# Kernel optimization log

Hardware: AMD Instinct MI355X
Metric: run time of the kernel (lower is better)

Reference implementation:

```python
import jax, jax.numpy as jnp
import numpy as np

B, S, H, F, E, TOP_K = 4, 2048, 768, 3072, 8, 2


def setup_inputs() -> dict:
    key = jax.random.key(0)
    ks = jax.random.split(key, 6)
    x = jax.random.normal(ks[0], (B, S, H), dtype=jnp.float32)
    Wr = jax.random.normal(ks[1], (E, H), dtype=jnp.float32) * 0.02
    Wi = jax.random.normal(ks[2], (E, F, H), dtype=jnp.float32) * 0.02
    bi = jnp.zeros((E, F), dtype=jnp.float32)
    Wo = jax.random.normal(ks[3], (E, H, F), dtype=jnp.float32) * 0.02
    bo = jnp.zeros((E, H), dtype=jnp.float32)
    return {"x": x, "Wr": Wr, "Wi": Wi, "bi": bi, "Wo": Wo, "bo": bo}


def reference(x, Wr, Wi, bi, Wo, bo):
    # x: [B, S, H] -> tokens [T, H]
    xf = x.reshape(-1, x.shape[-1])  # [T, H]

    # Router: linear (no bias), eval mode (no noise), temperature=1.0
    router_logits = jnp.einsum('th,eh->te', xf, Wr)  # [T, E]
    topk_vals, topk_idx = jax.lax.top_k(router_logits, TOP_K)  # [T, K]
    routing_weights = jax.nn.softmax(topk_vals, axis=-1)  # normalize over top-k

    # All experts on all tokens (forward_all_experts, parallel computation)
    h = jnp.einsum('th,efh->etf', xf, Wi) + bi[:, None, :]  # [E, T, F]
    h = jax.nn.gelu(h, approximate=False)  # BERT gelu (erf)
    expert_out = jnp.einsum('etf,ehf->eth', h, Wo) + bo[:, None, :]  # [E, T, H]
    expert_out = jnp.transpose(expert_out, (1, 0, 2))  # [T, E, H]

    # Gather top-k expert outputs per token and combine with routing weights
    gathered = jnp.take_along_axis(expert_out, topk_idx[:, :, None], axis=1)  # [T, K, H]
    out = jnp.einsum('tk,tkh->th', routing_weights, gathered)
    return out.reshape(x.shape)
```

## Files before the change

kernel.cpp:

```cpp
#include <hip/hip_runtime.h>
#include <hip/hip_bf16.h>
#include <cstdint>
#include <cstddef>

#define T_TOK 8192
#define HDIM  768
#define FDIM  3072
#define NEXP  8

typedef __attribute__((ext_vector_type(8))) __bf16 bf16x8;
typedef __attribute__((ext_vector_type(4))) float  f32x4;

static __device__ __forceinline__ f32x4 mfma16(bf16x8 a, bf16x8 b, f32x4 c) {
  return __builtin_amdgcn_mfma_f32_16x16x32_bf16(a, b, c, 0, 0, 0);
}

static __device__ __forceinline__ unsigned short f2b(float f) {
  return __builtin_bit_cast(unsigned short, (__bf16)f);
}

static constexpr size_t OFF_XB   = 0;
static constexpr size_t OFF_WIB  = OFF_XB  + (size_t)T_TOK * HDIM * 2;
static constexpr size_t OFF_WOB  = OFF_WIB + (size_t)NEXP * FDIM * HDIM * 2;
static constexpr size_t OFF_HBUF = OFF_WOB + (size_t)NEXP * HDIM * FDIM * 2;
static constexpr size_t OFF_META = OFF_HBUF + (size_t)2 * T_TOK * FDIM * 2;
static constexpr size_t OFF_TOKE = OFF_META + 256;
static constexpr size_t OFF_TOKW = OFF_TOKE + 65536;
static constexpr size_t OFF_PTOK = OFF_TOKW + 65536;
static constexpr size_t OFF_PW   = OFF_PTOK + 65536;
static constexpr size_t OFF_STAGE = 0;

__global__ __launch_bounds__(256) void cvt_kernel(const float* __restrict__ s,
                                                  unsigned short* __restrict__ d, int n4) {
  int i = blockIdx.x * 256 + threadIdx.x;
  int stride = gridDim.x * 256;
  for (; i < n4; i += stride) {
    float4 v = ((const float4*)s)[i];
    ushort4 o;
    o.x = f2b(v.x); o.y = f2b(v.y); o.z = f2b(v.z); o.w = f2b(v.w);
    ((ushort4*)d)[i] = o;
  }
}

__global__ __launch_bounds__(256) void router_kernel(const float* __restrict__ x,
                                                     const float* __restrict__ Wr,
                                                     int* __restrict__ tok_e,
                                                     float* __restrict__ tok_w) {
  __shared__ float wr[NEXP * HDIM];
  int tid = threadIdx.x;
  for (int i = tid; i < NEXP * HDIM; i += 256) wr[i] = Wr[i];
  __syncthreads();
  int lane = tid & 63;
  int wv = tid >> 6;
  int t = blockIdx.x * 4 + wv;
  const float* xr = x + (size_t)t * HDIM;
  float p[NEXP];
#pragma unroll
  for (int e = 0; e < NEXP; ++e) p[e] = 0.f;
  for (int j = 0; j < HDIM / 64; ++j) {
    float xv = xr[j * 64 + lane];
#pragma unroll
    for (int e = 0; e < NEXP; ++e) p[e] += xv * wr[e * HDIM + j * 64 + lane];
  }
#pragma unroll
  for (int e = 0; e < NEXP; ++e) {
    float v = p[e];
    for (int off = 32; off; off >>= 1) v += __shfl_xor(v, off);
    p[e] = v;
  }
  if (lane == 0) {
    float v0 = -1e30f, v1 = -1e30f; int i0 = 0, i1 = 0;
#pragma unroll
    for (int e = 0; e < NEXP; ++e) {
      float v = p[e];
      if (v > v0) { v1 = v0; i1 = i0; v0 = v; i0 = e; }
      else if (v > v1) { v1 = v; i1 = e; }
    }
    float ew = expf(v1 - v0);
    float w0 = 1.0f / (1.0f + ew);
    float w1 = ew * w0;
    tok_e[t * 2 + 0] = i0; tok_w[t * 2 + 0] = w0;
    tok_e[t * 2 + 1] = i1; tok_w[t * 2 + 1] = w1;
  }
}

__global__ __launch_bounds__(256) void count_kernel(const int* __restrict__ tok_e,
                                                    int* __restrict__ counts) {
  __shared__ int h[NEXP];
  int tid = threadIdx.x;
  if (tid < NEXP) h[tid] = 0;
  __syncthreads();
  int i = blockIdx.x * 256 + tid;
  atomicAdd(&h[tok_e[i]], 1);
  __syncthreads();
  if (tid < NEXP && h[tid] > 0) atomicAdd(&counts[tid], h[tid]);
}

__global__ void scan_kernel(const int* __restrict__ counts, int* __restrict__ base) {
  if (threadIdx.x == 0 && blockIdx.x == 0) {
    int s = 0;
    for (int e = 0; e < NEXP; ++e) { base[e] = s; s += counts[e]; }
  }
}

__global__ __launch_bounds__(256) void scatter_kernel(const int* __restrict__ tok_e,
                                                      const float* __restrict__ tok_w,
                                                      const int* __restrict__ base,
                                                      int* __restrict__ cursor,
                                                      int* __restrict__ pair_tok,
                                                      float* __restrict__ pair_w) {
  __shared__ int h[NEXP], bstart[NEXP];
  int tid = threadIdx.x;
  if (tid < NEXP) h[tid] = 0;
  __syncthreads();
  int i = blockIdx.x * 256 + tid;
  int e = tok_e[i];
  int r = atomicAdd(&h[e], 1);
  __syncthreads();
  if (tid < NEXP) bstart[tid] = (h[tid] > 0) ? atomicAdd(&cursor[tid], h[tid]) : 0;
  __syncthreads();
  int pos = base[e] + bstart[e] + r;
  pair_tok[pos] = i;
  pair_w[pos] = tok_w[i];
}

template <int MODE>
__global__ __launch_bounds__(512, 2) void moe_gemm(
    const unsigned short* __restrict__ abase,
    const unsigned short* __restrict__ wbase,
    const float* __restrict__ bias,
    const int* __restrict__ counts, const int* __restrict__ base,
    const int* __restrict__ pair_tok, const float* __restrict__ pair_w,
    unsigned short* __restrict__ hbuf, float* __restrict__ stage) {
  constexpr int K  = MODE ? FDIM : HDIM;
  constexpr int N  = MODE ? HDIM : FDIM;
  constexpr int NT = K / 64;

  const int e = blockIdx.z;
  const int ne = counts[e];
  const int mt = blockIdx.y;
  if (mt * 256 >= ne) return;
  const int nt = blockIdx.x;
  const int pb = base[e];

  extern __shared__ char smem[];

  const int tid = threadIdx.x;
  const int lane = tid & 63;
  const int wv = tid >> 6;
  const int wm = wv >> 2;
  const int wn = wv & 3;
  const int l15 = lane & 15;
  const int lkb = (lane >> 4) * 16;

  const int crow = tid >> 3;
  const int ck = tid & 7;
  const int swz = (ck ^ (crow & 7)) * 16;
  const char* aS[4]; const char* bS[4];
#pragma unroll
  for (int i = 0; i < 4; ++i) {
    int gr = mt * 256 + i * 64 + crow; if (gr > ne - 1) gr = ne - 1;
    if constexpr (MODE == 0) {
      int tok = pair_tok[pb + gr] >> 1;
      aS[i] = (const char*)abase + (size_t)tok * (HDIM * 2) + swz;
    } else {
      aS[i] = (const char*)abase + (size_t)(pb + gr) * (FDIM * 2) + swz;
    }
    int br = nt * 256 + i * 64 + crow;
    bS[i] = (const char*)wbase + ((size_t)e * N * K + (size_t)br * K) * 2 + swz;
  }

  auto STAGE = [&](int c, int t) {
    if (t < NT) {
      const char* src = (c < 4 ? aS[c] : bS[c - 4]) + t * 128;
      char* dst = smem + (size_t)((t & 1) * 65536 + c * 8192 + tid * 16);
      __builtin_amdgcn_global_load_lds(
          (const __attribute__((address_space(1))) void*)src,
          (__attribute__((address_space(3))) void*)dst, 16, 0, 0);
    }
  };

  bf16x8 aR[8], bR0[4], bR1[4];
  f32x4 acc[8][4];
#pragma unroll
  for (int mi = 0; mi < 8; ++mi)
#pragma unroll
    for (int ni = 0; ni < 4; ++ni) acc[mi][ni] = (f32x4){0.f, 0.f, 0.f, 0.f};

  auto READA = [&](int cb, int h) {
#pragma unroll
    for (int m2 = 0; m2 < 4; ++m2)
#pragma unroll
      for (int k2 = 0; k2 < 2; ++k2) {
        int lr = wm * 128 + (h * 4 + m2) * 16 + l15;
        int cbyte = k2 * 64 + lkb;
        aR[m2 * 2 + k2] =
            *(const bf16x8*)(smem + cb + lr * 128 + (cbyte ^ ((lr & 7) << 4)));
      }
  };
  auto READB = [&](int cb, int h, bf16x8* bR) {
#pragma unroll
    for (int n2 = 0; n2 < 2; ++n2)
#pragma unroll
      for (int k2 = 0; k2 < 2; ++k2) {
        int lr = wn * 64 + (h * 2 + n2) * 16 + l15;
        int cbyte = k2 * 64 + lkb;
        bR[n2 * 2 + k2] =
            *(const bf16x8*)(smem + cb + 32768 + lr * 128 + (cbyte ^ ((lr & 7) << 4)));
      }
  };
  auto MFMAQ = [&](int qm, int qn, const bf16x8* bR) {
#pragma unroll
    for (int m2 = 0; m2 < 4; ++m2)
#pragma unroll
      for (int n2 = 0; n2 < 2; ++n2)
#pragma unroll
        for (int k2 = 0; k2 < 2; ++k2)
          acc[qm * 4 + m2][qn * 2 + n2] =
              mfma16(aR[m2 * 2 + k2], bR[n2 * 2 + k2], acc[qm * 4 + m2][qn * 2 + n2]);
  };

#pragma unroll
  for (int c = 0; c < 8; ++c) STAGE(c, 0);
  STAGE(0, 1); STAGE(1, 1);
  asm volatile("s_waitcnt vmcnt(2)" ::: "memory");
  __builtin_amdgcn_s_barrier();

  for (int t = 0; t < NT; ++t) {
    const int cb = (t & 1) * 65536;
    READA(cb, 0); READB(cb, 0, bR0);
    STAGE(2, t + 1); STAGE(3, t + 1);
    __builtin_amdgcn_s_barrier();
    asm volatile("s_waitcnt lgkmcnt(0)" ::: "memory");
    __builtin_amdgcn_sched_barrier(0);
    __builtin_amdgcn_s_setprio(1);
    MFMAQ(0, 0, bR0);
    __builtin_amdgcn_s_setprio(0);
    __builtin_amdgcn_s_barrier();
    READB(cb, 1, bR1);
    STAGE(4, t + 1); STAGE(5, t + 1);
    __builtin_amdgcn_s_barrier();
    asm volatile("s_waitcnt lgkmcnt(0)" ::: "memory");
    __builtin_amdgcn_sched_barrier(0);
    __builtin_amdgcn_s_setprio(1);
    MFMAQ(0, 1, bR1);
    __builtin_amdgcn_s_setprio(0);
    __builtin_amdgcn_s_barrier();
    READA(cb, 1);
    STAGE(6, t + 1); STAGE(7, t + 1);
    __builtin_amdgcn_s_barrier();
    asm volatile("s_waitcnt lgkmcnt(0)" ::: "memory");
    __builtin_amdgcn_sched_barrier(0);
    __builtin_amdgcn_s_setprio(1);
    MFMAQ(1, 1, bR1);
    __builtin_amdgcn_s_setprio(0);
    __builtin_amdgcn_s_barrier();
    STAGE(0, t + 2); STAGE(1, t + 2);
    __builtin_amdgcn_s_barrier();
    __builtin_amdgcn_s_setprio(1);
    MFMAQ(1, 0, bR0);
    __builtin_amdgcn_s_setprio(0);
    if (t + 2 < NT) asm volatile("s_waitcnt vmcnt(2)" ::: "memory");
    else            asm volatile("s_waitcnt vmcnt(0)" ::: "memory");
    __builtin_amdgcn_s_barrier();
  }

  if constexpr (MODE == 0) {
    const float* be = bias + (size_t)e * FDIM;
    float bv[4];
#pragma unroll
    for (int ni = 0; ni < 4; ++ni) bv[ni] = be[nt * 256 + wn * 64 + ni * 16 + l15];
#pragma unroll
    for (int mi = 0; mi < 8; ++mi)
#pragma unroll
      for (int r = 0; r < 4; ++r) {
        int row = mt * 256 + wm * 128 + mi * 16 + (lane >> 4) * 4 + r;
        if (row < ne) {
          unsigned short* hr = hbuf + (size_t)(pb + row) * FDIM + nt * 256 + wn * 64 + l15;
#pragma unroll
          for (int ni = 0; ni < 4; ++ni) {
            float v = acc[mi][ni][r] + bv[ni];
            v = 0.5f * v * (1.0f + erff(v * 0.70710678118654752f));
            hr[ni * 16] = f2b(v);
          }
        }
      }
  } else {
    const float* be = bias + (size_t)e * HDIM;
    float bv[4];
#pragma unroll
    for (int ni = 0; ni < 4; ++ni) bv[ni] = be[nt * 256 + wn * 64 + ni * 16 + l15];
#pragma unroll
    for (int mi = 0; mi < 8; ++mi)
#pragma unroll
      for (int r = 0; r < 4; ++r) {
        int row = mt * 256 + wm * 128 + mi * 16 + (lane >> 4) * 4 + r;
        if (row < ne) {
          int p = pb + row;
          int ts = pair_tok[p];
          float w = pair_w[p];
          float* sr = stage + (size_t)ts * HDIM + nt * 256 + wn * 64 + l15;
#pragma unroll
          for (int ni = 0; ni < 4; ++ni)
            sr[ni * 16] = (acc[mi][ni][r] + bv[ni]) * w;
        }
      }
  }
}

__global__ __launch_bounds__(256) void combine_kernel(const float* __restrict__ stage,
                                                      float* __restrict__ out) {
  const int n4 = T_TOK * HDIM / 4;
  int i = blockIdx.x * 256 + threadIdx.x;
  int stride = gridDim.x * 256;
  const float4* s = (const float4*)stage;
  float4* o = (float4*)out;
  for (; i < n4; i += stride) {
    int t = i / (HDIM / 4);
    int h = i - t * (HDIM / 4);
    float4 a = s[(size_t)t * (HDIM / 2) + h];
    float4 b = s[(size_t)t * (HDIM / 2) + (HDIM / 4) + h];
    float4 r; r.x = a.x + b.x; r.y = a.y + b.y; r.z = a.z + b.z; r.w = a.w + b.w;
    o[i] = r;
  }
}

extern "C" void kernel_launch(void* const* d_in, const int* in_sizes, int n_in,
                              void* d_out, int out_size, void* d_ws, size_t ws_size,
                              hipStream_t stream) {
  const float* x  = (const float*)d_in[0];
  const float* Wr = (const float*)d_in[1];
  const float* Wi = (const float*)d_in[2];
  const float* bi = (const float*)d_in[3];
  const float* Wo = (const float*)d_in[4];
  const float* bo = (const float*)d_in[5];
  float* out = (float*)d_out;
  char* ws = (char*)d_ws;

  unsigned short* xb   = (unsigned short*)(ws + OFF_XB);
  unsigned short* wib  = (unsigned short*)(ws + OFF_WIB);
  unsigned short* wob  = (unsigned short*)(ws + OFF_WOB);
  unsigned short* hbuf = (unsigned short*)(ws + OFF_HBUF);
  int*   counts   = (int*)(ws + OFF_META);
  int*   basep    = (int*)(ws + OFF_META + 64);
  int*   cursor   = (int*)(ws + OFF_META + 128);
  int*   tok_e    = (int*)(ws + OFF_TOKE);
  float* tok_w    = (float*)(ws + OFF_TOKW);
  int*   pair_tok = (int*)(ws + OFF_PTOK);
  float* pair_w   = (float*)(ws + OFF_PW);
  float* stage    = (float*)(ws + OFF_STAGE);

  hipFuncSetAttribute((const void*)&moe_gemm<0>,
                      hipFuncAttributeMaxDynamicSharedMemorySize, 131072);
  hipFuncSetAttribute((const void*)&moe_gemm<1>,
                      hipFuncAttributeMaxDynamicSharedMemorySize, 131072);

  hipMemsetAsync(ws + OFF_META, 0, 256, stream);

  cvt_kernel<<<1024, 256, 0, stream>>>(x, xb, T_TOK * HDIM / 4);
  cvt_kernel<<<2048, 256, 0, stream>>>(Wi, wib, NEXP * FDIM * HDIM / 4);
  cvt_kernel<<<2048, 256, 0, stream>>>(Wo, wob, NEXP * HDIM * FDIM / 4);

  router_kernel<<<T_TOK / 4, 256, 0, stream>>>(x, Wr, tok_e, tok_w);
  count_kernel<<<64, 256, 0, stream>>>(tok_e, counts);
  scan_kernel<<<1, 64, 0, stream>>>(counts, basep);
  scatter_kernel<<<64, 256, 0, stream>>>(tok_e, tok_w, basep, cursor, pair_tok, pair_w);

  moe_gemm<0><<<dim3(FDIM / 256, T_TOK / 256, NEXP), 512, 131072, stream>>>(
      xb, wib, bi, counts, basep, pair_tok, pair_w, hbuf, nullptr);
  moe_gemm<1><<<dim3(HDIM / 256, T_TOK / 256, NEXP), 512, 131072, stream>>>(
      hbuf, wob, bo, counts, basep, pair_tok, pair_w, nullptr, stage);

  combine_kernel<<<2048, 256, 0, stream>>>(stage, out);
}
```

Before: 332.6 us.

## Split MoE GEMM into specialized kernels with 256x192 tiles and swizzled block order

Replaces the templated grouped GEMM with two dedicated kernels. The down-projection now uses 256x192 output tiles, so each expert gets four N tiles instead of three and more workgroups run on the many-CU GPU. It uses a reduced shared-memory footprint and a new MFMA schedule split into 2+1 column subgroups. Both kernels use 1-D grids with experts interleaved and M tiles grouped for L2 reuse of weights and activations. The cost is a narrower N tile with less reuse of A per block and a more complex pipeline.

```diff
diff --git a/kernel.cpp b/kernel.cpp
--- a/kernel.cpp
+++ b/kernel.cpp
@@ -17,6 +17,12 @@
 
 static __device__ __forceinline__ unsigned short f2b(float f) {
   return __builtin_bit_cast(unsigned short, (__bf16)f);
+}
+
+static __device__ __forceinline__ void gload16(const void* g, void* l) {
+  __builtin_amdgcn_global_load_lds(
+      (const __attribute__((address_space(1))) void*)g,
+      (__attribute__((address_space(3))) void*)l, 16, 0, 0);
 }
 
 static constexpr size_t OFF_XB   = 0;
@@ -124,24 +130,22 @@
   pair_w[pos] = tok_w[i];
 }
 
-template <int MODE>
-__global__ __launch_bounds__(512, 2) void moe_gemm(
-    const unsigned short* __restrict__ abase,
-    const unsigned short* __restrict__ wbase,
-    const float* __restrict__ bias,
+__global__ __launch_bounds__(512, 2) void gemmA_kernel(
+    const unsigned short* __restrict__ xb, const unsigned short* __restrict__ wib,
+    const float* __restrict__ bi,
     const int* __restrict__ counts, const int* __restrict__ base,
-    const int* __restrict__ pair_tok, const float* __restrict__ pair_w,
-    unsigned short* __restrict__ hbuf, float* __restrict__ stage) {
-  constexpr int K  = MODE ? FDIM : HDIM;
-  constexpr int N  = MODE ? HDIM : FDIM;
-  constexpr int NT = K / 64;
-
-  const int e = blockIdx.z;
+    const int* __restrict__ pair_tok, unsigned short* __restrict__ hbuf) {
+  const int bid = blockIdx.x;
+  const int e = bid & 7;
+  const int j = bid >> 3;
+  const int mtq = j / 48;
+  const int rem = j - mtq * 48;
+  const int nt = rem >> 2;
+  const int mt = mtq * 4 + (rem & 3);
   const int ne = counts[e];
-  const int mt = blockIdx.y;
   if (mt * 256 >= ne) return;
-  const int nt = blockIdx.x;
   const int pb = base[e];
+  constexpr int NT = HDIM / 64;
 
   extern __shared__ char smem[];
 
@@ -160,23 +164,17 @@
 #pragma unroll
   for (int i = 0; i < 4; ++i) {
     int gr = mt * 256 + i * 64 + crow; if (gr > ne - 1) gr = ne - 1;
-    if constexpr (MODE == 0) {
-      int tok = pair_tok[pb + gr] >> 1;
-      aS[i] = (const char*)abase + (size_t)tok * (HDIM * 2) + swz;
-    } else {
-      aS[i] = (const char*)abase + (size_t)(pb + gr) * (FDIM * 2) + swz;
-    }
+    int tok = pair_tok[pb + gr] >> 1;
+    aS[i] = (const char*)xb + (size_t)tok * (HDIM * 2) + swz;
     int br = nt * 256 + i * 64 + crow;
-    bS[i] = (const char*)wbase + ((size_t)e * N * K + (size_t)br * K) * 2 + swz;
+    bS[i] = (const char*)wib + ((size_t)e * FDIM * HDIM + (size_t)br * HDIM) * 2 + swz;
   }
 
   auto STAGE = [&](int c, int t) {
     if (t < NT) {
       const char* src = (c < 4 ? aS[c] : bS[c - 4]) + t * 128;
       char* dst = smem + (size_t)((t & 1) * 65536 + c * 8192 + tid * 16);
-      __builtin_amdgcn_global_load_lds(
-          (const __attribute__((address_space(1))) void*)src,
-          (__attribute__((address_space(3))) void*)dst, 16, 0, 0);
+      gload16(src, dst);
     }
   };
 
@@ -265,47 +263,196 @@
     __builtin_amdgcn_s_barrier();
   }
 
-  if constexpr (MODE == 0) {
-    const float* be = bias + (size_t)e * FDIM;
-    float bv[4];
-#pragma unroll
-    for (int ni = 0; ni < 4; ++ni) bv[ni] = be[nt * 256 + wn * 64 + ni * 16 + l15];
-#pragma unroll
-    for (int mi = 0; mi < 8; ++mi)
-#pragma unroll
-      for (int r = 0; r < 4; ++r) {
-        int row = mt * 256 + wm * 128 + mi * 16 + (lane >> 4) * 4 + r;
-        if (row < ne) {
-          unsigned short* hr = hbuf + (size_t)(pb + row) * FDIM + nt * 256 + wn * 64 + l15;
-#pragma unroll
-          for (int ni = 0; ni < 4; ++ni) {
-            float v = acc[mi][ni][r] + bv[ni];
-            v = 0.5f * v * (1.0f + erff(v * 0.70710678118654752f));
-            hr[ni * 16] = f2b(v);
-          }
+  const float* be = bi + (size_t)e * FDIM;
+  float bv[4];
+#pragma unroll
+  for (int ni = 0; ni < 4; ++ni) bv[ni] = be[nt * 256 + wn * 64 + ni * 16 + l15];
+#pragma unroll
+  for (int mi = 0; mi < 8; ++mi)
+#pragma unroll
+    for (int r = 0; r < 4; ++r) {
+      int row = mt * 256 + wm * 128 + mi * 16 + (lane >> 4) * 4 + r;
+      if (row < ne) {
+        unsigned short* hr = hbuf + (size_t)(pb + row) * FDIM + nt * 256 + wn * 64 + l15;
+#pragma unroll
+        for (int ni = 0; ni < 4; ++ni) {
+          float v = acc[mi][ni][r] + bv[ni];
+          v = 0.5f * v * (1.0f + erff(v * 0.70710678118654752f));
+          hr[ni * 16] = f2b(v);
         }
       }
-  } else {
-    const float* be = bias + (size_t)e * HDIM;
-    float bv[4];
-#pragma unroll
-    for (int ni = 0; ni < 4; ++ni) bv[ni] = be[nt * 256 + wn * 64 + ni * 16 + l15];
-#pragma unroll
-    for (int mi = 0; mi < 8; ++mi)
-#pragma unroll
-      for (int r = 0; r < 4; ++r) {
-        int row = mt * 256 + wm * 128 + mi * 16 + (lane >> 4) * 4 + r;
-        if (row < ne) {
-          int p = pb + row;
-          int ts = pair_tok[p];
-          float w = pair_w[p];
-          float* sr = stage + (size_t)ts * HDIM + nt * 256 + wn * 64 + l15;
-#pragma unroll
-          for (int ni = 0; ni < 4; ++ni)
-            sr[ni * 16] = (acc[mi][ni][r] + bv[ni]) * w;
-        }
+    }
+}
+
+__global__ __launch_bounds__(512, 2) void gemmB_kernel(
+    const unsigned short* __restrict__ hbuf, const unsigned short* __restrict__ wob,
+    const float* __restrict__ bo,
+    const int* __restrict__ counts, const int* __restrict__ base,
+    const int* __restrict__ pair_tok, const float* __restrict__ pair_w,
+    float* __restrict__ stage) {
+  const int bid = blockIdx.x;
+  const int e = bid & 7;
+  const int j = bid >> 3;
+  const int mt = j >> 2;
+  const int nt = j & 3;
+  const int ne = counts[e];
+  if (mt * 256 >= ne) return;
+  const int pb = base[e];
+  constexpr int NT = FDIM / 64;
+  constexpr int BUFS = 57344;
+
+  extern __shared__ char smem[];
+
+  const int tid = threadIdx.x;
+  const int lane = tid & 63;
+  const int wv = tid >> 6;
+  const int wm = wv >> 2;
+  const int wn = wv & 3;
+  const int l15 = lane & 15;
+  const int lkb = (lane >> 4) * 16;
+
+  const int crow = tid >> 3;
+  const int ck = tid & 7;
+  const int swz = (ck ^ (crow & 7)) * 16;
+  const char* aS[4]; const char* bS[3];
+#pragma unroll
+  for (int i = 0; i < 4; ++i) {
+    int gr = mt * 256 + i * 64 + crow; if (gr > ne - 1) gr = ne - 1;
+    aS[i] = (const char*)hbuf + (size_t)(pb + gr) * (FDIM * 2) + swz;
+  }
+#pragma unroll
+  for (int i = 0; i < 3; ++i) {
+    int br = nt * 192 + i * 64 + crow;
+    bS[i] = (const char*)wob + ((size_t)e * HDIM * FDIM + (size_t)br * FDIM) * 2 + swz;
+  }
+
+  auto STAGE = [&](int c, int t) {
+    if (t < NT) {
+      const char* src = (c < 4 ? aS[c] : bS[c - 4]) + t * 128;
+      char* dst = smem + (size_t)((t & 1) * BUFS +
+                                  (c < 4 ? c * 8192 : 32768 + (c - 4) * 8192) + tid * 16);
+      gload16(src, dst);
+    }
+  };
+
+  bf16x8 aR[8], b01[4], b2[2];
+  f32x4 acc[8][3];
+#pragma unroll
+  for (int mi = 0; mi < 8; ++mi)
+#pragma unroll
+    for (int ni = 0; ni < 3; ++ni) acc[mi][ni] = (f32x4){0.f, 0.f, 0.f, 0.f};
+
+  auto READA = [&](int cb, int h) {
+#pragma unroll
+    for (int m2 = 0; m2 < 4; ++m2)
+#pragma unroll
+      for (int k2 = 0; k2 < 2; ++k2) {
+        int lr = wm * 128 + (h * 4 + m2) * 16 + l15;
+        int cbyte = k2 * 64 + lkb;
+        aR[m2 * 2 + k2] =
+            *(const bf16x8*)(smem + cb + lr * 128 + (cbyte ^ ((lr & 7) << 4)));
       }
-  }
+  };
+  auto READB01 = [&](int cb) {
+#pragma unroll
+    for (int n2 = 0; n2 < 2; ++n2)
+#pragma unroll
+      for (int k2 = 0; k2 < 2; ++k2) {
+        int lr = wn * 48 + n2 * 16 + l15;
+        int cbyte = k2 * 64 + lkb;
+        b01[n2 * 2 + k2] =
+            *(const bf16x8*)(smem + cb + 32768 + lr * 128 + (cbyte ^ ((lr & 7) << 4)));
+      }
+  };
+  auto READB2 = [&](int cb) {
+#pragma unroll
+    for (int k2 = 0; k2 < 2; ++k2) {
+      int lr = wn * 48 + 32 + l15;
+      int cbyte = k2 * 64 + lkb;
+      b2[k2] = *(const bf16x8*)(smem + cb + 32768 + lr * 128 + (cbyte ^ ((lr & 7) << 4)));
+    }
+  };
+  auto Q01 = [&](int h) {
+#pragma unroll
+    for (int m2 = 0; m2 < 4; ++m2)
+#pragma unroll
+      for (int n2 = 0; n2 < 2; ++n2)
+#pragma unroll
+        for (int k2 = 0; k2 < 2; ++k2)
+          acc[h * 4 + m2][n2] = mfma16(aR[m2 * 2 + k2], b01[n2 * 2 + k2], acc[h * 4 + m2][n2]);
+  };
+  auto Q2 = [&](int h) {
+#pragma unroll
+    for (int m2 = 0; m2 < 4; ++m2)
+#pragma unroll
+      for (int k2 = 0; k2 < 2; ++k2)
+        acc[h * 4 + m2][2] = mfma16(aR[m2 * 2 + k2], b2[k2], acc[h * 4 + m2][2]);
+  };
+
+#pragma unroll
+  for (int c = 0; c < 7; ++c) STAGE(c, 0);
+  STAGE(0, 1); STAGE(1, 1);
+  asm volatile("s_waitcnt vmcnt(2)" ::: "memory");
+  __builtin_amdgcn_s_barrier();
+
+  for (int t = 0; t < NT; ++t) {
+    const int cb = (t & 1) * BUFS;
+    READA(cb, 0); READB01(cb);
+    STAGE(2, t + 1); STAGE(3, t + 1);
+    __builtin_amdgcn_s_barrier();
+    asm volatile("s_waitcnt lgkmcnt(0)" ::: "memory");
+    __builtin_amdgcn_sched_barrier(0);
+    __builtin_amdgcn_s_setprio(1);
+    Q01(0);
+    __builtin_amdgcn_s_setprio(0);
+    __builtin_amdgcn_s_barrier();
+    READB2(cb);
+    STAGE(4, t + 1); STAGE(5, t + 1);
+    __builtin_amdgcn_s_barrier();
+    asm volatile("s_waitcnt lgkmcnt(0)" ::: "memory");
+    __builtin_amdgcn_sched_barrier(0);
+    __builtin_amdgcn_s_setprio(1);
+    Q2(0);
+    __builtin_amdgcn_s_setprio(0);
+    __builtin_amdgcn_s_barrier();
+    READA(cb, 1);
+    STAGE(6, t + 1);
+    __builtin_amdgcn_s_barrier();
+    asm volatile("s_waitcnt lgkmcnt(0)" ::: "memory");
+    __builtin_amdgcn_sched_barrier(0);
+    __builtin_amdgcn_s_setprio(1);
+    Q2(1);
+    __builtin_amdgcn_s_setprio(0);
+    __builtin_amdgcn_s_barrier();
+    STAGE(0, t + 2); STAGE(1, t + 2);
+    __builtin_amdgcn_s_barrier();
+    __builtin_amdgcn_s_setprio(1);
+    Q01(1);
+    __builtin_amdgcn_s_setprio(0);
+    if (t + 2 < NT) asm volatile("s_waitcnt vmcnt(2)" ::: "memory");
+    else            asm volatile("s_waitcnt vmcnt(0)" ::: "memory");
+    __builtin_amdgcn_s_barrier();
+  }
+
+  const float* be = bo + (size_t)e * HDIM;
+  float bv[3];
+#pragma unroll
+  for (int ni = 0; ni < 3; ++ni) bv[ni] = be[nt * 192 + wn * 48 + ni * 16 + l15];
+#pragma unroll
+  for (int mi = 0; mi < 8; ++mi)
+#pragma unroll
+    for (int r = 0; r < 4; ++r) {
+      int row = mt * 256 + wm * 128 + mi * 16 + (lane >> 4) * 4 + r;
+      if (row < ne) {
+        int p = pb + row;
+        int ts = pair_tok[p];
+        float w = pair_w[p];
+        float* sr = stage + (size_t)ts * HDIM + nt * 192 + wn * 48 + l15;
+#pragma unroll
+        for (int ni = 0; ni < 3; ++ni)
+          sr[ni * 16] = (acc[mi][ni][r] + bv[ni]) * w;
+      }
+    }
 }
 
 __global__ __launch_bounds__(256) void combine_kernel(const float* __restrict__ stage,
@@ -350,10 +497,10 @@
   float* pair_w   = (float*)(ws + OFF_PW);
   float* stage    = (float*)(ws + OFF_STAGE);
 
-  hipFuncSetAttribute((const void*)&moe_gemm<0>,
+  hipFuncSetAttribute((const void*)&gemmA_kernel,
                       hipFuncAttributeMaxDynamicSharedMemorySize, 131072);
-  hipFuncSetAttribute((const void*)&moe_gemm<1>,
-                      hipFuncAttributeMaxDynamicSharedMemorySize, 131072);
+  hipFuncSetAttribute((const void*)&gemmB_kernel,
+                      hipFuncAttributeMaxDynamicSharedMemorySize, 114688);
 
   hipMemsetAsync(ws + OFF_META, 0, 256, stream);
 
@@ -366,10 +513,10 @@
   scan_kernel<<<1, 64, 0, stream>>>(counts, basep);
   scatter_kernel<<<64, 256, 0, stream>>>(tok_e, tok_w, basep, cursor, pair_tok, pair_w);
 
-  moe_gemm<0><<<dim3(FDIM / 256, T_TOK / 256, NEXP), 512, 131072, stream>>>(
-      xb, wib, bi, counts, basep, pair_tok, pair_w, hbuf, nullptr);
-  moe_gemm<1><<<dim3(HDIM / 256, T_TOK / 256, NEXP), 512, 131072, stream>>>(
-      hbuf, wob, bo, counts, basep, pair_tok, pair_w, nullptr, stage);
+  gemmA_kernel<<<8 * 32 * 12, 512, 131072, stream>>>(
+      xb, wib, bi, counts, basep, pair_tok, hbuf);
+  gemmB_kernel<<<8 * 32 * 4, 512, 114688, stream>>>(
+      hbuf, wob, bo, counts, basep, pair_tok, pair_w, stage);
 
   combine_kernel<<<2048, 256, 0, stream>>>(stage, out);
 }
```

New measurement: 400.9 us. 20.5% more time.

## Schedule MoE GEMM tiles from a compact XCD-grouped list; use tanh GELU

Applied to the files above, without the earlier changes.

The scan kernel now also builds a compact list of (expert, m-tile) pairs. Both expert GEMMs launch a 1D grid that reads this list. Blocks are mapped so each XCD (blockIdx.x & 7) takes a contiguous run of tiles, keeping tiles of the same expert together for better L2 reuse of weights and activations. This replaces the old 3D grid, where most blocks exited early. Separately, the erf-based GELU epilogue is replaced by a tanh approximation built from exp2 and rcp intrinsics, which is cheaper but deviates slightly from the exact erf reference.

```diff
diff --git a/kernel.cpp b/kernel.cpp
--- a/kernel.cpp
+++ b/kernel.cpp
@@ -17,6 +17,16 @@
 
 static __device__ __forceinline__ unsigned short f2b(float f) {
   return __builtin_bit_cast(unsigned short, (__bf16)f);
+}
+
+static __device__ __forceinline__ float gelu_f(float x) {
+  float x2 = x * x;
+  float y = x * (0.7978845608f + 0.0356774081f * x2);
+  float ay = __builtin_fabsf(y);
+  float z = __builtin_amdgcn_exp2f(ay * -2.885390082f);
+  float t = (1.0f - z) * __builtin_amdgcn_rcpf(1.0f + z);
+  t = __builtin_copysignf(t, y);
+  return 0.5f * x * (1.0f + t);
 }
 
 static constexpr size_t OFF_XB   = 0;
@@ -28,6 +38,7 @@
 static constexpr size_t OFF_TOKW = OFF_TOKE + 65536;
 static constexpr size_t OFF_PTOK = OFF_TOKW + 65536;
 static constexpr size_t OFF_PW   = OFF_PTOK + 65536;
+static constexpr size_t OFF_TILE = OFF_PW + 65536;
 static constexpr size_t OFF_STAGE = 0;
 
 __global__ __launch_bounds__(256) void cvt_kernel(const float* __restrict__ s,
@@ -96,11 +107,18 @@
   if (tid < NEXP && h[tid] > 0) atomicAdd(&counts[tid], h[tid]);
 }
 
-__global__ void scan_kernel(const int* __restrict__ counts, int* __restrict__ base) {
-  if (threadIdx.x == 0 && blockIdx.x == 0) {
-    int s = 0;
-    for (int e = 0; e < NEXP; ++e) { base[e] = s; s += counts[e]; }
-  }
+__global__ void scan_build_kernel(const int* __restrict__ counts, int* __restrict__ basep,
+                                  int* __restrict__ tile_e, int* __restrict__ tile_mt,
+                                  int* __restrict__ ntiles) {
+  if (threadIdx.x != 0 || blockIdx.x != 0) return;
+  int s = 0;
+  for (int e = 0; e < NEXP; ++e) { basep[e] = s; s += counts[e]; }
+  int n = 0;
+  for (int e = 0; e < NEXP; ++e) {
+    int nmt = (counts[e] + 255) >> 8;
+    for (int m = 0; m < nmt; ++m) { tile_e[n] = e; tile_mt[n] = m; ++n; }
+  }
+  ntiles[0] = n;
 }
 
 __global__ __launch_bounds__(256) void scatter_kernel(const int* __restrict__ tok_e,
@@ -131,16 +149,26 @@
     const float* __restrict__ bias,
     const int* __restrict__ counts, const int* __restrict__ base,
     const int* __restrict__ pair_tok, const float* __restrict__ pair_w,
+    const int* __restrict__ tile_e, const int* __restrict__ tile_mt,
+    const int* __restrict__ ntiles,
     unsigned short* __restrict__ hbuf, float* __restrict__ stage) {
-  constexpr int K  = MODE ? FDIM : HDIM;
-  constexpr int N  = MODE ? HDIM : FDIM;
-  constexpr int NT = K / 64;
-
-  const int e = blockIdx.z;
+  constexpr int K   = MODE ? FDIM : HDIM;
+  constexpr int N   = MODE ? HDIM : FDIM;
+  constexpr int NT  = K / 64;
+  constexpr int NTC = N / 256;
+
+  const int xcd = blockIdx.x & 7;
+  const int slot = blockIdx.x >> 3;
+  const int mtl = slot / NTC;
+  const int nt = slot - mtl * NTC;
+  const int ntl = ntiles[0];
+  const int q = ntl >> 3, r = ntl & 7;
+  const int cnt = q + (xcd < r ? 1 : 0);
+  if (mtl >= cnt) return;
+  const int gt = xcd * q + (xcd < r ? xcd : r) + mtl;
+  const int e = tile_e[gt];
+  const int mt = tile_mt[gt];
   const int ne = counts[e];
-  const int mt = blockIdx.y;
-  if (mt * 256 >= ne) return;
-  const int nt = blockIdx.x;
   const int pb = base[e];
 
   extern __shared__ char smem[];
@@ -273,16 +301,13 @@
 #pragma unroll
     for (int mi = 0; mi < 8; ++mi)
 #pragma unroll
-      for (int r = 0; r < 4; ++r) {
-        int row = mt * 256 + wm * 128 + mi * 16 + (lane >> 4) * 4 + r;
+      for (int rr = 0; rr < 4; ++rr) {
+        int row = mt * 256 + wm * 128 + mi * 16 + (lane >> 4) * 4 + rr;
         if (row < ne) {
           unsigned short* hr = hbuf + (size_t)(pb + row) * FDIM + nt * 256 + wn * 64 + l15;
 #pragma unroll
-          for (int ni = 0; ni < 4; ++ni) {
-            float v = acc[mi][ni][r] + bv[ni];
-            v = 0.5f * v * (1.0f + erff(v * 0.70710678118654752f));
-            hr[ni * 16] = f2b(v);
-          }
+          for (int ni = 0; ni < 4; ++ni)
+            hr[ni * 16] = f2b(gelu_f(acc[mi][ni][rr] + bv[ni]));
         }
       }
   } else {
@@ -293,8 +318,8 @@
 #pragma unroll
     for (int mi = 0; mi < 8; ++mi)
 #pragma unroll
-      for (int r = 0; r < 4; ++r) {
-        int row = mt * 256 + wm * 128 + mi * 16 + (lane >> 4) * 4 + r;
+      for (int rr = 0; rr < 4; ++rr) {
+        int row = mt * 256 + wm * 128 + mi * 16 + (lane >> 4) * 4 + rr;
         if (row < ne) {
           int p = pb + row;
           int ts = pair_tok[p];
@@ -302,7 +327,7 @@
           float* sr = stage + (size_t)ts * HDIM + nt * 256 + wn * 64 + l15;
 #pragma unroll
           for (int ni = 0; ni < 4; ++ni)
-            sr[ni * 16] = (acc[mi][ni][r] + bv[ni]) * w;
+            sr[ni * 16] = (acc[mi][ni][rr] + bv[ni]) * w;
         }
       }
   }
@@ -320,8 +345,8 @@
     int h = i - t * (HDIM / 4);
     float4 a = s[(size_t)t * (HDIM / 2) + h];
     float4 b = s[(size_t)t * (HDIM / 2) + (HDIM / 4) + h];
-    float4 r; r.x = a.x + b.x; r.y = a.y + b.y; r.z = a.z + b.z; r.w = a.w + b.w;
-    o[i] = r;
+    float4 rr; rr.x = a.x + b.x; rr.y = a.y + b.y; rr.z = a.z + b.z; rr.w = a.w + b.w;
+    o[i] = rr;
   }
 }
 
@@ -348,6 +373,9 @@
   float* tok_w    = (float*)(ws + OFF_TOKW);
   int*   pair_tok = (int*)(ws + OFF_PTOK);
   float* pair_w   = (float*)(ws + OFF_PW);
+  int*   tile_e   = (int*)(ws + OFF_TILE);
+  int*   tile_mt  = (int*)(ws + OFF_TILE + 512);
+  int*   ntiles   = (int*)(ws + OFF_TILE + 1024);
   float* stage    = (float*)(ws + OFF_STAGE);
 
   hipFuncSetAttribute((const void*)&moe_gemm<0>,
@@ -363,13 +391,13 @@
 
   router_kernel<<<T_TOK / 4, 256, 0, stream>>>(x, Wr, tok_e, tok_w);
   count_kernel<<<64, 256, 0, stream>>>(tok_e, counts);
-  scan_kernel<<<1, 64, 0, stream>>>(counts, basep);
+  scan_build_kernel<<<1, 64, 0, stream>>>(counts, basep, tile_e, tile_mt, ntiles);
   scatter_kernel<<<64, 256, 0, stream>>>(tok_e, tok_w, basep, cursor, pair_tok, pair_w);
 
-  moe_gemm<0><<<dim3(FDIM / 256, T_TOK / 256, NEXP), 512, 131072, stream>>>(
-      xb, wib, bi, counts, basep, pair_tok, pair_w, hbuf, nullptr);
-  moe_gemm<1><<<dim3(HDIM / 256, T_TOK / 256, NEXP), 512, 131072, stream>>>(
-      hbuf, wob, bo, counts, basep, pair_tok, pair_w, nullptr, stage);
+  moe_gemm<0><<<8 * 9 * (FDIM / 256), 512, 131072, stream>>>(
+      xb, wib, bi, counts, basep, pair_tok, pair_w, tile_e, tile_mt, ntiles, hbuf, nullptr);
+  moe_gemm<1><<<8 * 9 * (HDIM / 256), 512, 131072, stream>>>(
+      hbuf, wob, bo, counts, basep, pair_tok, pair_w, tile_e, tile_mt, ntiles, nullptr, stage);
 
   combine_kernel<<<2048, 256, 0, stream>>>(stage, out);
 }
```

Result: faster. 300.5 us (-9.7%).
